# Optimization experiments

Measured on AMD Instinct MI355X. Metric: run time of the kernel, lower is better.

Reference implementation:

```python
import jax, jax.numpy as jnp
import numpy as np

B, S, D = 4, 2048, 1024  # batch, seq_len, d_model (h=16 but unused due to source bug)


def setup_inputs() -> dict:
    key = jax.random.key(0)
    ks = jax.random.split(key, 12)
    scale = 1.0 / np.sqrt(D)
    return {
        "q": jax.random.normal(ks[0], (B, S, D), jnp.float32),
        "k": jax.random.normal(ks[1], (B, S, D), jnp.float32),
        "v": jax.random.normal(ks[2], (B, S, D), jnp.float32),
        "mask": jnp.ones((1, 1, S, S), dtype=bool),
        "Wq": jax.random.normal(ks[3], (D, D), jnp.float32) * scale,
        "bq": jnp.zeros((D,), jnp.float32),
        "Wk": jax.random.normal(ks[4], (D, D), jnp.float32) * scale,
        "bk": jnp.zeros((D,), jnp.float32),
        "Wv": jax.random.normal(ks[5], (D, D), jnp.float32) * scale,
        "bv": jnp.zeros((D,), jnp.float32),
        "Wo": jax.random.normal(ks[6], (D, D), jnp.float32) * scale,
        "bo": jnp.zeros((D,), jnp.float32),
    }


def reference(q, k, v, mask, Wq, bq, Wk, bk, Wv, bv, Wo, bo):
    # Faithful to source bugs: head split discarded (attention over full d_model),
    # mask discarded (masked_fill out-of-place), dropout=0 (identity).
    query = q @ Wq + bq  # [B,S,D]
    key = k @ Wk + bk
    value = v @ Wv + bv
    d_k = query.shape[-1]  # = d_model due to the bug
    scores = jnp.einsum('bqd,bkd->bqk', query, key) / jnp.sqrt(jnp.float32(d_k))
    attn = jax.nn.softmax(scores, axis=-1)  # [B,S,S]
    x = jnp.einsum('bqk,bkd->bqd', attn, value)  # [B,S,D]
    # source: x.transpose(1,2).contiguous().view(B,-1,D) -> layout permutation
    b, s, d = x.shape
    x = jnp.swapaxes(x, 1, 2).reshape(b, s, d)
    return x @ Wo + bo
```

## Files before the change

kernel.cpp:

```cpp
#include <hip/hip_runtime.h>
#include <hip/hip_bf16.h>
#include <stdint.h>

typedef __attribute__((ext_vector_type(8))) short short8;
typedef __attribute__((ext_vector_type(4))) float f32x4;
typedef const __attribute__((address_space(1))) uint32_t* gas1_t;
typedef __attribute__((address_space(3))) uint32_t* las3_t;

__device__ __forceinline__ short f2bf(float f) {
  uint32_t u = __builtin_bit_cast(uint32_t, f);
  u += 0x7fffu + ((u >> 16) & 1u);
  return (short)(u >> 16);
}
__device__ __forceinline__ float bf2f(short s) {
  return __builtin_bit_cast(float, ((uint32_t)(uint16_t)s) << 16);
}

__global__ __launch_bounds__(256) void cvt_qkv_k(const float* __restrict__ q,
    const float* __restrict__ k, const float* __restrict__ v,
    short* __restrict__ dst) {
  const long long n = 8388608LL;
  const float* src = (blockIdx.z == 0) ? q : (blockIdx.z == 1) ? k : v;
  long long i = ((long long)blockIdx.x * 256 + threadIdx.x) * 8;
  float4 a = *(const float4*)(src + i);
  float4 b = *(const float4*)(src + i + 4);
  short8 o;
  o[0]=f2bf(a.x); o[1]=f2bf(a.y); o[2]=f2bf(a.z); o[3]=f2bf(a.w);
  o[4]=f2bf(b.x); o[5]=f2bf(b.y); o[6]=f2bf(b.z); o[7]=f2bf(b.w);
  *(short8*)(dst + (long long)blockIdx.z * n + i) = o;
}

__global__ __launch_bounds__(256) void bias_gather_k(const float* b0, const float* b1,
    const float* b2, const float* b3, float* __restrict__ dst) {
  int i = blockIdx.x * 256 + threadIdx.x;
  if (i >= 4096) return;
  int z = i >> 10, j = i & 1023;
  const float* s = (z==0)?b0:(z==1)?b1:(z==2)?b2:b3;
  dst[i] = s[j];
}

__global__ __launch_bounds__(256) void wt_cvt_k(const float* w0, const float* w1,
    const float* w2, const float* w3, short* __restrict__ dst) {
  __shared__ float t[32][33];
  const float* W = (blockIdx.z==0)?w0:(blockIdx.z==1)?w1:(blockIdx.z==2)?w2:w3;
  short* D = dst + (long long)blockIdx.z * 1048576LL;
  int n0 = blockIdx.x * 32, k0 = blockIdx.y * 32;
  int tx = threadIdx.x, ty = threadIdx.y;
  #pragma unroll
  for (int i = 0; i < 4; ++i)
    t[ty + 8*i][tx] = W[(long long)(k0 + ty + 8*i) * 1024 + n0 + tx];
  __syncthreads();
  #pragma unroll
  for (int i = 0; i < 4; ++i)
    D[(long long)(n0 + ty + 8*i) * 1024 + k0 + tx] = f2bf(t[tx][ty + 8*i]);
}

__global__ __launch_bounds__(256) void tr_bf16_k(const short* __restrict__ in,
    short* __restrict__ out, long long sIn, long long sOut) {
  __shared__ short t[32][33];
  in  += (long long)blockIdx.z * sIn;
  out += (long long)blockIdx.z * sOut;
  int c0 = blockIdx.x * 32, r0 = blockIdx.y * 32;
  int tx = threadIdx.x, ty = threadIdx.y;
  #pragma unroll
  for (int i = 0; i < 4; ++i)
    t[ty + 8*i][tx] = in[(long long)(r0 + ty + 8*i) * 1024 + c0 + tx];
  __syncthreads();
  #pragma unroll
  for (int i = 0; i < 4; ++i)
    out[(long long)(c0 + ty + 8*i) * 2048 + r0 + tx] = t[tx][ty + 8*i];
}

__global__ __launch_bounds__(256) void softmax_bf_k(short* __restrict__ SP) {
  short* sp = SP + (long long)blockIdx.x * 2048;
  const int t = threadIdx.x;
  short8 sv = *(const short8*)(sp + t*8);
  float v[8];
  #pragma unroll
  for (int j = 0; j < 8; ++j) v[j] = bf2f(sv[j]);
  float m = v[0];
  #pragma unroll
  for (int j = 1; j < 8; ++j) m = fmaxf(m, v[j]);
  #pragma unroll
  for (int off = 32; off > 0; off >>= 1) m = fmaxf(m, __shfl_down(m, off, 64));
  __shared__ float rmax[4], rsum[4];
  int wv = t >> 6, ln = t & 63;
  if (ln == 0) rmax[wv] = m;
  __syncthreads();
  m = fmaxf(fmaxf(rmax[0], rmax[1]), fmaxf(rmax[2], rmax[3]));
  float e[8], sum = 0.f;
  #pragma unroll
  for (int j = 0; j < 8; ++j) { e[j] = exp2f((v[j] - m) * 1.44269504f); sum += e[j]; }
  #pragma unroll
  for (int off = 32; off > 0; off >>= 1) sum += __shfl_down(sum, off, 64);
  if (ln == 0) rsum[wv] = sum;
  __syncthreads();
  float inv = 1.0f / (rsum[0] + rsum[1] + rsum[2] + rsum[3]);
  short8 o;
  #pragma unroll
  for (int j = 0; j < 8; ++j) o[j] = f2bf(e[j] * inv);
  *(short8*)(sp + t*8) = o;
}

#define MFMA16(d, a_, b_) d = __builtin_amdgcn_mfma_f32_16x16x32_bf16(a_, b_, d, 0, 0, 0)
#define LGKM0 do { asm volatile("s_waitcnt lgkmcnt(0)" ::: "memory"); \
                   __builtin_amdgcn_sched_barrier(0); } while (0)
#define XCD_DECODE(gxs_, gys_) \
  const int nwg = (int)gridDim.x; \
  const int wg = ((int)blockIdx.x & 7) * (nwg >> 3) + ((int)blockIdx.x >> 3); \
  const int bxi = wg & ((1 << (gxs_)) - 1); \
  const int byi = (wg >> (gxs_)) & ((1 << (gys_)) - 1); \
  const int z = wg >> ((gxs_) + (gys_));

template<int OUT_BF16>
__global__ __launch_bounds__(512, 2) void gemm8_k(const short* __restrict__ A,
    const short* __restrict__ Bt, void* __restrict__ Cv,
    const float* __restrict__ bias,
    int M, int N, int K, long long sA, long long sB, long long sC,
    long long sBias, float scale, int gxs, int gys)
{
  __shared__ __align__(16) short lds[2][2][256*64];
  XCD_DECODE(gxs, gys);
  A  += (long long)z * sA;
  Bt += (long long)z * sB;
  const int bm = byi * 256;
  const int bn = bxi * 256;
  const int tid  = threadIdx.x;
  const int w    = tid >> 6, lane = tid & 63;
  const int wr   = w >> 2,   wc   = w & 3;
  const int lr   = lane & 15, lk  = lane >> 4;

  const int rsw0 = ((lk    ) ^ (lr & 7)) * 8;
  const int rsw1 = ((lk + 4) ^ (lr & 7)) * 8;
  const int srow = w * 8 + (lane >> 3);
  const int swc  = ((lane & 7) ^ ((lane >> 3) & 7)) * 8;
  const short* gA[4]; const short* gB[4];
  #pragma unroll
  for (int i = 0; i < 4; ++i) {
    gA[i] = A  + (long long)(bm + i*64 + srow) * K + swc;
    gB[i] = Bt + (long long)(bn + i*64 + srow) * K + swc;
  }

  #define STG(buf, ab, i, kt) \
    __builtin_amdgcn_global_load_lds((gas1_t)(((ab) ? gB : gA)[i] + (long long)(kt)*64), \
        (las3_t)&lds[buf][ab][(i)*4096 + w*512], 16, 0, 0)
  #define RDA(buf, mi, ks) (*(const short8*)&lds[buf][0][(wr*128 + (mi)*16 + lr)*64 + ((ks) ? rsw1 : rsw0)])
  #define RDB(buf, ni, ks) (*(const short8*)&lds[buf][1][(wc*64  + (ni)*16 + lr)*64 + ((ks) ? rsw1 : rsw0)])

  f32x4 acc[8][4] = {};
  const int nt = K >> 6;

  #pragma unroll
  for (int i = 0; i < 4; ++i) STG(0, 0, i, 0);
  #pragma unroll
  for (int i = 0; i < 4; ++i) STG(0, 1, i, 0);
  STG(1, 0, 0, 1); STG(1, 0, 2, 1);
  STG(1, 1, 0, 1); STG(1, 1, 1, 1);
  STG(1, 1, 2, 1); STG(1, 1, 3, 1);
  asm volatile("s_waitcnt vmcnt(6)" ::: "memory");
  __builtin_amdgcn_s_barrier();

  for (int g = 0; g < nt; ++g) {
    const int b = g & 1, nb = b ^ 1;
    short8 aR[4][2], bR[4][2];
    #pragma unroll
    for (int mi = 0; mi < 4; ++mi) { aR[mi][0] = RDA(b, mi, 0); aR[mi][1] = RDA(b, mi, 1); }
    #pragma unroll
    for (int ni = 0; ni < 2; ++ni) { bR[ni][0] = RDB(b, ni, 0); bR[ni][1] = RDB(b, ni, 1); }
    if (g + 1 < nt) { STG(nb, 0, 1, g+1); STG(nb, 0, 3, g+1); }
    __builtin_amdgcn_s_barrier();
    LGKM0;
    __builtin_amdgcn_s_setprio(1);
    #pragma unroll
    for (int mi = 0; mi < 4; ++mi)
      #pragma unroll
      for (int ni = 0; ni < 2; ++ni) {
        MFMA16(acc[mi][ni], aR[mi][0], bR[ni][0]);
        MFMA16(acc[mi][ni], aR[mi][1], bR[ni][1]);
      }
    __builtin_amdgcn_s_setprio(0);
    __builtin_amdgcn_s_barrier();
    #pragma unroll
    for (int ni = 2; ni < 4; ++ni) { bR[ni][0] = RDB(b, ni, 0); bR[ni][1] = RDB(b, ni, 1); }
    if (g + 2 < nt) { STG(b, 0, 0, g+2); STG(b, 0, 2, g+2); }
    __builtin_amdgcn_s_barrier();
    LGKM0;
    __builtin_amdgcn_s_setprio(1);
    #pragma unroll
    for (int mi = 0; mi < 4; ++mi)
      #pragma unroll
      for (int ni = 2; ni < 4; ++ni) {
        MFMA16(acc[mi][ni], aR[mi][0], bR[ni][0]);
        MFMA16(acc[mi][ni], aR[mi][1], bR[ni][1]);
      }
    __builtin_amdgcn_s_setprio(0);
    __builtin_amdgcn_s_barrier();
    #pragma unroll
    for (int mi = 0; mi < 4; ++mi) { aR[mi][0] = RDA(b, mi+4, 0); aR[mi][1] = RDA(b, mi+4, 1); }
    if (g + 2 < nt) { STG(b, 1, 0, g+2); STG(b, 1, 1, g+2); }
    __builtin_amdgcn_s_barrier();
    LGKM0;
    __builtin_amdgcn_s_setprio(1);
    #pragma unroll
    for (int mi = 0; mi < 4; ++mi)
      #pragma unroll
      for (int ni = 0; ni < 2; ++ni) {
        MFMA16(acc[mi+4][ni], aR[mi][0], bR[ni][0]);
        MFMA16(acc[mi+4][ni], aR[mi][1], bR[ni][1]);
      }
    __builtin_amdgcn_s_setprio(0);
    __builtin_amdgcn_s_barrier();
    if (g + 2 < nt) { STG(b, 1, 2, g+2); STG(b, 1, 3, g+2); }
    __builtin_amdgcn_s_setprio(1);
    #pragma unroll
    for (int mi = 0; mi < 4; ++mi)
      #pragma unroll
      for (int ni = 2; ni < 4; ++ni) {
        MFMA16(acc[mi+4][ni], aR[mi][0], bR[ni][0]);
        MFMA16(acc[mi+4][ni], aR[mi][1], bR[ni][1]);
      }
    __builtin_amdgcn_s_setprio(0);
    if (g + 1 < nt) {
      if (g + 2 < nt) asm volatile("s_waitcnt vmcnt(6)" ::: "memory");
      else            asm volatile("s_waitcnt vmcnt(0)" ::: "memory");
    }
    __builtin_amdgcn_s_barrier();
  }

  const float* bz = bias ? (bias + (long long)z * sBias) : nullptr;
  #pragma unroll
  for (int mi = 0; mi < 8; ++mi) {
    const int row = bm + wr*128 + mi*16 + lk*4;
    #pragma unroll
    for (int ni = 0; ni < 4; ++ni) {
      const int col = bn + wc*64 + ni*16 + lr;
      const float bval = bz ? bz[col] : 0.f;
      #pragma unroll
      for (int r = 0; r < 4; ++r) {
        float val = acc[mi][ni][r] * scale + bval;
        if (OUT_BF16)
          ((short*)Cv)[(long long)z*sC + (long long)(row + r) * N + col] = f2bf(val);
        else
          ((float*)Cv)[(long long)z*sC + (long long)(row + r) * N + col] = val;
      }
    }
  }
  #undef STG
  #undef RDA
  #undef RDB
}

template<int OUT_BF16>
__global__ __launch_bounds__(512, 2) void gemm4_k(const short* __restrict__ A,
    const short* __restrict__ Bt, void* __restrict__ Cv,
    const float* __restrict__ bias,
    int M, int N, int K, long long sA, long long sB, long long sC,
    long long sBias, float scale, int gxs, int gys)
{
  __shared__ __align__(16) short lds[2][24576];
  XCD_DECODE(gxs, gys);
  A  += (long long)z * sA;
  Bt += (long long)z * sB;
  const int bm = byi * 256;
  const int bn = bxi * 128;
  const int tid  = threadIdx.x;
  const int w    = tid >> 6, lane = tid & 63;
  const int wr   = w >> 2,   wc   = w & 3;
  const int lr   = lane & 15, lk  = lane >> 4;

  const int rsw0 = ((lk    ) ^ (lr & 7)) * 8;
  const int rsw1 = ((lk + 4) ^ (lr & 7)) * 8;
  const int srow = w * 8 + (lane >> 3);
  const int swc  = ((lane & 7) ^ ((lane >> 3) & 7)) * 8;
  const short* gA[4]; const short* gB[2];
  #pragma unroll
  for (int i = 0; i < 4; ++i)
    gA[i] = A + (long long)(bm + i*64 + srow) * K + swc;
  #pragma unroll
  for (int i = 0; i < 2; ++i)
    gB[i] = Bt + (long long)(bn + i*64 + srow) * K + swc;

  #define STGA(buf, i, kt) \
    __builtin_amdgcn_global_load_lds((gas1_t)(gA[i] + (long long)(kt)*64), \
        (las3_t)&lds[buf][(i)*4096 + w*512], 16, 0, 0)
  #define STGB(buf, i, kt) \
    __builtin_amdgcn_global_load_lds((gas1_t)(gB[i] + (long long)(kt)*64), \
        (las3_t)&lds[buf][16384 + (i)*4096 + w*512], 16, 0, 0)
  #define RDA4(buf, mi, ks) (*(const short8*)&lds[buf][(wr*128 + (mi)*16 + lr)*64 + ((ks) ? rsw1 : rsw0)])
  #define RDB4(buf, ni, ks) (*(const short8*)&lds[buf][16384 + (wc*32 + (ni)*16 + lr)*64 + ((ks) ? rsw1 : rsw0)])

  f32x4 acc[8][2] = {};
  const int nt = K >> 6;

  STGA(0, 0, 0); STGA(0, 2, 0); STGB(0, 0, 0); STGB(0, 1, 0);
  STGA(0, 1, 0); STGA(0, 3, 0);
  asm volatile("s_waitcnt vmcnt(2)" ::: "memory");
  __builtin_amdgcn_s_barrier();

  for (int g = 0; g < nt; ++g) {
    const int b = g & 1, nb = b ^ 1;
    short8 aR[4][2], bR[2][2];
    #pragma unroll
    for (int mi = 0; mi < 4; ++mi) { aR[mi][0] = RDA4(b, mi, 0); aR[mi][1] = RDA4(b, mi, 1); }
    #pragma unroll
    for (int ni = 0; ni < 2; ++ni) { bR[ni][0] = RDB4(b, ni, 0); bR[ni][1] = RDB4(b, ni, 1); }
    if (g + 1 < nt) { STGA(nb, 0, g+1); STGA(nb, 2, g+1); STGB(nb, 0, g+1); STGB(nb, 1, g+1); }
    __builtin_amdgcn_s_barrier();
    LGKM0;
    __builtin_amdgcn_s_setprio(1);
    #pragma unroll
    for (int mi = 0; mi < 4; ++mi)
      #pragma unroll
      for (int ni = 0; ni < 2; ++ni) {
        MFMA16(acc[mi][ni], aR[mi][0], bR[ni][0]);
        MFMA16(acc[mi][ni], aR[mi][1], bR[ni][1]);
      }
    __builtin_amdgcn_s_setprio(0);
    if (g + 1 < nt) asm volatile("s_waitcnt vmcnt(4)" ::: "memory");
    else            asm volatile("s_waitcnt vmcnt(0)" ::: "memory");
    __builtin_amdgcn_s_barrier();
    #pragma unroll
    for (int mi = 0; mi < 4; ++mi) { aR[mi][0] = RDA4(b, mi+4, 0); aR[mi][1] = RDA4(b, mi+4, 1); }
    if (g + 1 < nt) { STGA(nb, 1, g+1); STGA(nb, 3, g+1); }
    __builtin_amdgcn_s_barrier();
    LGKM0;
    __builtin_amdgcn_s_setprio(1);
    #pragma unroll
    for (int mi = 0; mi < 4; ++mi)
      #pragma unroll
      for (int ni = 0; ni < 2; ++ni) {
        MFMA16(acc[mi+4][ni], aR[mi][0], bR[ni][0]);
        MFMA16(acc[mi+4][ni], aR[mi][1], bR[ni][1]);
      }
    __builtin_amdgcn_s_setprio(0);
    if (g + 1 < nt) asm volatile("s_waitcnt vmcnt(2)" ::: "memory");
    __builtin_amdgcn_s_barrier();
  }

  const float* bz = bias ? (bias + (long long)z * sBias) : nullptr;
  #pragma unroll
  for (int mi = 0; mi < 8; ++mi) {
    const int row = bm + wr*128 + mi*16 + lk*4;
    #pragma unroll
    for (int ni = 0; ni < 2; ++ni) {
      const int col = bn + wc*32 + ni*16 + lr;
      const float bval = bz ? bz[col] : 0.f;
      #pragma unroll
      for (int r = 0; r < 4; ++r) {
        float val = acc[mi][ni][r] * scale + bval;
        if (OUT_BF16)
          ((short*)Cv)[(long long)z*sC + (long long)(row + r) * N + col] = f2bf(val);
        else
          ((float*)Cv)[(long long)z*sC + (long long)(row + r) * N + col] = val;
      }
    }
  }
  #undef STGA
  #undef STGB
  #undef RDA4
  #undef RDB4
}

extern "C" void kernel_launch(void* const* d_in, const int* in_sizes, int n_in,
                              void* d_out, int out_size, void* d_ws, size_t ws_size,
                              hipStream_t stream) {
  const float* q  = (const float*)d_in[0];
  const float* k  = (const float*)d_in[1];
  const float* v  = (const float*)d_in[2];
  const float* Wq = (const float*)d_in[4];
  const float* bq = (const float*)d_in[5];
  const float* Wk = (const float*)d_in[6];
  const float* bk = (const float*)d_in[7];
  const float* Wv = (const float*)d_in[8];
  const float* bv = (const float*)d_in[9];
  const float* Wo = (const float*)d_in[10];
  const float* bo = (const float*)d_in[11];

  char* w = (char*)d_ws;
  short* Wt     = (short*)(w);
  float* biasb  = (float*)(w + 8388608);
  short* QKV    = (short*)(w + 8404992);
  short* qkvbf  = (short*)(w + 58736640);
  short* P      = (short*)(w + 58736640);
  short* x      = (short*)(w + 92291072);
  short* Vt     = (short*)(w + 109068288);
  short* xt     = (short*)(w + 125845504);

  short* Qp = QKV;
  short* Kp = QKV + 8388608LL;
  short* Vp = QKV + 16777216LL;

  cvt_qkv_k<<<dim3(4096,1,3), 256, 0, stream>>>(q, k, v, qkvbf);
  bias_gather_k<<<dim3(16), 256, 0, stream>>>(bq, bk, bv, bo, biasb);
  wt_cvt_k<<<dim3(32,32,4), dim3(32,8), 0, stream>>>(Wq, Wk, Wv, Wo, Wt);

  gemm4_k<1><<<768, 512, 0, stream>>>(qkvbf, Wt, QKV, biasb,
      8192, 1024, 1024, 8388608LL, 1048576LL, 8388608LL, 1024LL, 1.0f, 3, 5);

  tr_bf16_k<<<dim3(32,64,4), dim3(32,8), 0, stream>>>(Vp, Vt, 2097152LL, 2097152LL);

  gemm8_k<1><<<256, 512, 0, stream>>>(Qp, Kp, P, nullptr,
      2048, 2048, 1024, 2097152LL, 2097152LL, 4194304LL, 0LL, 0.03125f, 3, 3);

  softmax_bf_k<<<dim3(8192), 256, 0, stream>>>(P);

  gemm4_k<1><<<256, 512, 0, stream>>>(P, Vt, x, nullptr,
      2048, 1024, 2048, 4194304LL, 2097152LL, 2097152LL, 0LL, 1.0f, 3, 3);

  tr_bf16_k<<<dim3(32,64,4), dim3(32,8), 0, stream>>>(x, xt, 2097152LL, 2097152LL);

  gemm4_k<0><<<256, 512, 0, stream>>>(xt, Wt + 3145728LL, (float*)d_out,
      biasb + 3072, 2048, 1024, 1024, 2097152LL, 0LL, 2097152LL, 0LL, 1.0f, 3, 3);
}
```

Before: 239.5 us.

## Compute V and attention output transposed to drop both transpose kernels; triple-buffer gemm4

Computes V directly in transposed form as Wv^T·v^T with a row bias, and computes the attention output as Vt·P^T so it lands already in the permuted layout the output projection needs. This removes both bf16 transpose kernels and their extra memory round trips. The gemm4 kernel also moves from double to triple-buffered LDS with loads issued two tiles ahead and fewer barriers per iteration. The cost is more LDS per block, which may limit occupancy, and a strided B operand layout in the PV GEMM.

```diff
diff --git a/kernel.cpp b/kernel.cpp
--- a/kernel.cpp
+++ b/kernel.cpp
@@ -53,22 +53,6 @@
   #pragma unroll
   for (int i = 0; i < 4; ++i)
     D[(long long)(n0 + ty + 8*i) * 1024 + k0 + tx] = f2bf(t[tx][ty + 8*i]);
-}
-
-__global__ __launch_bounds__(256) void tr_bf16_k(const short* __restrict__ in,
-    short* __restrict__ out, long long sIn, long long sOut) {
-  __shared__ short t[32][33];
-  in  += (long long)blockIdx.z * sIn;
-  out += (long long)blockIdx.z * sOut;
-  int c0 = blockIdx.x * 32, r0 = blockIdx.y * 32;
-  int tx = threadIdx.x, ty = threadIdx.y;
-  #pragma unroll
-  for (int i = 0; i < 4; ++i)
-    t[ty + 8*i][tx] = in[(long long)(r0 + ty + 8*i) * 1024 + c0 + tx];
-  __syncthreads();
-  #pragma unroll
-  for (int i = 0; i < 4; ++i)
-    out[(long long)(c0 + ty + 8*i) * 2048 + r0 + tx] = t[tx][ty + 8*i];
 }
 
 __global__ __launch_bounds__(256) void softmax_bf_k(short* __restrict__ SP) {
@@ -250,14 +234,15 @@
   #undef RDB
 }
 
-template<int OUT_BF16>
+template<int OUT_BF16, int BIAS_ROW>
 __global__ __launch_bounds__(512, 2) void gemm4_k(const short* __restrict__ A,
     const short* __restrict__ Bt, void* __restrict__ Cv,
     const float* __restrict__ bias,
-    int M, int N, int K, long long sA, long long sB, long long sC,
-    long long sBias, float scale, int gxs, int gys)
+    int K, int lda, int ldb, int ldc,
+    long long sA, long long sB, long long sC, long long sBias,
+    float scale, int gxs, int gys)
 {
-  __shared__ __align__(16) short lds[2][24576];
+  __shared__ __align__(16) short lds[3][24576];
   XCD_DECODE(gxs, gys);
   A  += (long long)z * sA;
   Bt += (long long)z * sB;
@@ -275,10 +260,10 @@
   const short* gA[4]; const short* gB[2];
   #pragma unroll
   for (int i = 0; i < 4; ++i)
-    gA[i] = A + (long long)(bm + i*64 + srow) * K + swc;
+    gA[i] = A + (long long)(bm + i*64 + srow) * lda + swc;
   #pragma unroll
   for (int i = 0; i < 2; ++i)
-    gB[i] = Bt + (long long)(bn + i*64 + srow) * K + swc;
+    gB[i] = Bt + (long long)(bn + i*64 + srow) * ldb + swc;
 
   #define STGA(buf, i, kt) \
     __builtin_amdgcn_global_load_lds((gas1_t)(gA[i] + (long long)(kt)*64), \
@@ -292,20 +277,21 @@
   f32x4 acc[8][2] = {};
   const int nt = K >> 6;
 
-  STGA(0, 0, 0); STGA(0, 2, 0); STGB(0, 0, 0); STGB(0, 1, 0);
-  STGA(0, 1, 0); STGA(0, 3, 0);
-  asm volatile("s_waitcnt vmcnt(2)" ::: "memory");
+  STGA(0, 0, 0); STGA(0, 2, 0); STGB(0, 0, 0);
+  STGB(0, 1, 0); STGA(0, 1, 0); STGA(0, 3, 0);
+  STGA(1, 0, 1); STGA(1, 2, 1); STGB(1, 0, 1);
+  STGB(1, 1, 1); STGA(1, 1, 1); STGA(1, 3, 1);
+  asm volatile("s_waitcnt vmcnt(6)" ::: "memory");
   __builtin_amdgcn_s_barrier();
 
+  int b = 0, nb = 2;
   for (int g = 0; g < nt; ++g) {
-    const int b = g & 1, nb = b ^ 1;
     short8 aR[4][2], bR[2][2];
     #pragma unroll
     for (int mi = 0; mi < 4; ++mi) { aR[mi][0] = RDA4(b, mi, 0); aR[mi][1] = RDA4(b, mi, 1); }
     #pragma unroll
     for (int ni = 0; ni < 2; ++ni) { bR[ni][0] = RDB4(b, ni, 0); bR[ni][1] = RDB4(b, ni, 1); }
-    if (g + 1 < nt) { STGA(nb, 0, g+1); STGA(nb, 2, g+1); STGB(nb, 0, g+1); STGB(nb, 1, g+1); }
-    __builtin_amdgcn_s_barrier();
+    if (g + 2 < nt) { STGA(nb, 0, g+2); STGA(nb, 2, g+2); STGB(nb, 0, g+2); }
     LGKM0;
     __builtin_amdgcn_s_setprio(1);
     #pragma unroll
@@ -316,13 +302,9 @@
         MFMA16(acc[mi][ni], aR[mi][1], bR[ni][1]);
       }
     __builtin_amdgcn_s_setprio(0);
-    if (g + 1 < nt) asm volatile("s_waitcnt vmcnt(4)" ::: "memory");
-    else            asm volatile("s_waitcnt vmcnt(0)" ::: "memory");
-    __builtin_amdgcn_s_barrier();
     #pragma unroll
     for (int mi = 0; mi < 4; ++mi) { aR[mi][0] = RDA4(b, mi+4, 0); aR[mi][1] = RDA4(b, mi+4, 1); }
-    if (g + 1 < nt) { STGA(nb, 1, g+1); STGA(nb, 3, g+1); }
-    __builtin_amdgcn_s_barrier();
+    if (g + 2 < nt) { STGB(nb, 1, g+2); STGA(nb, 1, g+2); STGA(nb, 3, g+2); }
     LGKM0;
     __builtin_amdgcn_s_setprio(1);
     #pragma unroll
@@ -333,25 +315,29 @@
         MFMA16(acc[mi+4][ni], aR[mi][1], bR[ni][1]);
       }
     __builtin_amdgcn_s_setprio(0);
-    if (g + 1 < nt) asm volatile("s_waitcnt vmcnt(2)" ::: "memory");
-    __builtin_amdgcn_s_barrier();
-  }
-
-  const float* bz = bias ? (bias + (long long)z * sBias) : nullptr;
+    if (g + 2 < nt)      asm volatile("s_waitcnt vmcnt(6)" ::: "memory");
+    else if (g + 1 < nt) asm volatile("s_waitcnt vmcnt(0)" ::: "memory");
+    __builtin_amdgcn_s_barrier();
+    b  = (b  == 2) ? 0 : b  + 1;
+    nb = (nb == 2) ? 0 : nb + 1;
+  }
+
+  const float* bz = bias;
   #pragma unroll
   for (int mi = 0; mi < 8; ++mi) {
     const int row = bm + wr*128 + mi*16 + lk*4;
     #pragma unroll
     for (int ni = 0; ni < 2; ++ni) {
       const int col = bn + wc*32 + ni*16 + lr;
-      const float bval = bz ? bz[col] : 0.f;
+      const float bcol = (bz && !BIAS_ROW) ? bz[(long long)z*sBias + col] : 0.f;
       #pragma unroll
       for (int r = 0; r < 4; ++r) {
+        float bval = BIAS_ROW ? bz[row + r] : bcol;
         float val = acc[mi][ni][r] * scale + bval;
         if (OUT_BF16)
-          ((short*)Cv)[(long long)z*sC + (long long)(row + r) * N + col] = f2bf(val);
+          ((short*)Cv)[(long long)z*sC + (long long)(row + r) * ldc + col] = f2bf(val);
         else
-          ((float*)Cv)[(long long)z*sC + (long long)(row + r) * N + col] = val;
+          ((float*)Cv)[(long long)z*sC + (long long)(row + r) * ldc + col] = val;
       }
     }
   }
@@ -382,33 +368,31 @@
   short* QKV    = (short*)(w + 8404992);
   short* qkvbf  = (short*)(w + 58736640);
   short* P      = (short*)(w + 58736640);
-  short* x      = (short*)(w + 92291072);
-  short* Vt     = (short*)(w + 109068288);
-  short* xt     = (short*)(w + 125845504);
+  short* Vt     = (short*)(w + 92291072);
+  short* xt     = (short*)(w + 109068288);
 
   short* Qp = QKV;
   short* Kp = QKV + 8388608LL;
-  short* Vp = QKV + 16777216LL;
+  short* vbf = qkvbf + 16777216LL;
 
   cvt_qkv_k<<<dim3(4096,1,3), 256, 0, stream>>>(q, k, v, qkvbf);
   bias_gather_k<<<dim3(16), 256, 0, stream>>>(bq, bk, bv, bo, biasb);
   wt_cvt_k<<<dim3(32,32,4), dim3(32,8), 0, stream>>>(Wq, Wk, Wv, Wo, Wt);
 
-  gemm4_k<1><<<768, 512, 0, stream>>>(qkvbf, Wt, QKV, biasb,
-      8192, 1024, 1024, 8388608LL, 1048576LL, 8388608LL, 1024LL, 1.0f, 3, 5);
-
-  tr_bf16_k<<<dim3(32,64,4), dim3(32,8), 0, stream>>>(Vp, Vt, 2097152LL, 2097152LL);
+  gemm4_k<1,0><<<512, 512, 0, stream>>>(qkvbf, Wt, QKV, biasb,
+      1024, 1024, 1024, 1024, 8388608LL, 1048576LL, 8388608LL, 1024LL, 1.0f, 3, 5);
+
+  gemm4_k<1,1><<<256, 512, 0, stream>>>(Wt + 2097152LL, vbf, Vt, biasb + 2048,
+      1024, 1024, 1024, 8192, 0LL, 0LL, 0LL, 0LL, 1.0f, 6, 2);
 
   gemm8_k<1><<<256, 512, 0, stream>>>(Qp, Kp, P, nullptr,
       2048, 2048, 1024, 2097152LL, 2097152LL, 4194304LL, 0LL, 0.03125f, 3, 3);
 
   softmax_bf_k<<<dim3(8192), 256, 0, stream>>>(P);
 
-  gemm4_k<1><<<256, 512, 0, stream>>>(P, Vt, x, nullptr,
-      2048, 1024, 2048, 4194304LL, 2097152LL, 2097152LL, 0LL, 1.0f, 3, 3);
-
-  tr_bf16_k<<<dim3(32,64,4), dim3(32,8), 0, stream>>>(x, xt, 2097152LL, 2097152LL);
-
-  gemm4_k<0><<<256, 512, 0, stream>>>(xt, Wt + 3145728LL, (float*)d_out,
-      biasb + 3072, 2048, 1024, 1024, 2097152LL, 0LL, 2097152LL, 0LL, 1.0f, 3, 3);
-}
+  gemm4_k<1,0><<<256, 512, 0, stream>>>(Vt, P, xt, nullptr,
+      2048, 8192, 2048, 2048, 2048LL, 4194304LL, 2097152LL, 0LL, 1.0f, 4, 2);
+
+  gemm4_k<0,0><<<256, 512, 0, stream>>>(xt, Wt + 3145728LL, (float*)d_out,
+      biasb + 3072, 1024, 1024, 1024, 1024, 2097152LL, 0LL, 2097152LL, 0LL, 1.0f, 3, 3);
+}
```

Result: faster. 221.9 us (-7.4%).
